# Optimization experiments

Hardware: AMD Instinct MI355X
Metric: run time of the kernel (lower is better)

The kernel has to match this reference:

```python
import jax, jax.numpy as jnp
import numpy as np

WS = 7            # window_size
P = WS * WS       # tokens per window
NUM_HEADS = 12
N_SCALES = 3      # n_local_region_scales
LOCAL_HEAD = NUM_HEADS // N_SCALES

# relative position index (Swin-style), precomputed as a constant
_coords = np.stack(np.meshgrid(np.arange(WS), np.arange(WS), indexing='ij'))  # (2,WS,WS)
_cf = _coords.reshape(2, -1)                                                  # (2,P)
_rel = (_cf[:, :, None] - _cf[:, None, :]).transpose(1, 2, 0)                 # (P,P,2)
_rel[:, :, 0] += WS - 1
_rel[:, :, 1] += WS - 1
_rel[:, :, 0] *= 2 * WS - 1
REL_IDX = jnp.asarray(_rel.sum(-1))  # (P,P) int


def window_partition(arr, ws):
    # arr: (B, H, W, C) -> (B * H/ws * W/ws, ws, ws, C)
    B, H, W, C = arr.shape
    a = arr.reshape(B, H // ws, ws, W // ws, ws, C)
    return a.transpose(0, 1, 3, 2, 4, 5).reshape(-1, ws, ws, C)


def setup_inputs() -> dict:
    key = jax.random.key(0)
    ks = jax.random.split(key, 4)
    B, H, W, C = 16, 56, 56, 384
    N = H * W
    return {
        'x': jax.random.normal(ks[0], (B, N, C), dtype=jnp.float32),
        'w_qkv': jax.random.normal(ks[1], (C, 3 * C), dtype=jnp.float32) * 0.02,
        'w_proj': jax.random.normal(ks[2], (C, C), dtype=jnp.float32) * 0.02,
        'b_proj': jnp.zeros((C,), dtype=jnp.float32),
        'rel_bias_table': jax.random.normal(ks[3], ((2 * WS - 1) ** 2, LOCAL_HEAD), dtype=jnp.float32) * 0.02,
        'H': H,
        'W': W,
    }


def reference(x, w_qkv, w_proj, b_proj, rel_bias_table, H, W):
    B, N, C = x.shape
    head_dim = C // NUM_HEADS
    local_C = C // N_SCALES
    scale = head_dim ** -0.5

    # qkv projection (no bias), laid out as (3, B, N, C)
    temp = (x @ w_qkv).reshape(B, N, 3, C).transpose(2, 0, 1, 3)

    # relative position bias: (LOCAL_HEAD, P, P)
    bias = rel_bias_table[REL_IDX.reshape(-1)].reshape(P, P, LOCAL_HEAD).transpose(2, 0, 1)

    outs = []
    for i in range(N_SCALES):
        qkv = temp[:, :, :, i * local_C:(i + 1) * local_C]          # (3,B,N,local_C)
        oh, ow = H // (2 ** i), W // (2 ** i)
        n_region = (oh // WS) * (ow // WS)
        qkv = qkv.reshape(3 * B, N, local_C).transpose(0, 2, 1).reshape(3 * B, local_C, H, W)
        if i > 0:
            k = 2 ** i
            r = qkv.reshape(3 * B, local_C, oh, k, ow, k)
            qkv = r.mean(axis=(3, 5)) + r.max(axis=(3, 5))           # avg_pool + max_pool
        qkv = qkv.transpose(0, 2, 3, 1)                              # (3B, oh, ow, local_C)
        qkv = window_partition(qkv, WS)                              # (3B*n_region, WS, WS, local_C)
        qkv = qkv.reshape(3, B, n_region, WS, WS, LOCAL_HEAD, head_dim).transpose(0, 1, 5, 2, 3, 4, 6)
        # NOTE: the original reshapes (B,LOCAL_HEAD,n_region,WS,WS,hd) -> (-1,LOCAL_HEAD,P,hd),
        # which mixes batch/head/region axes; replicated faithfully (row-major reshape).
        q = qkv[0].reshape(-1, LOCAL_HEAD, P, head_dim)
        kk = qkv[1].reshape(-1, LOCAL_HEAD, P, head_dim)
        v = qkv[2].reshape(-1, LOCAL_HEAD, P, head_dim)
        attn = (q * scale) @ jnp.swapaxes(kk, -2, -1) + bias[None]   # (B*R, LH, P, P)
        attn = jax.nn.softmax(attn, axis=-1)
        y = attn @ v                                                 # (B*R, LH, P, hd)
        # faithful inverse of the mixed reshape + (non-inverse) window merge via plain reshape
        y = y.reshape(B, n_region, LOCAL_HEAD, P, head_dim).transpose(0, 2, 4, 1, 3)
        y = y.reshape(B, local_C, oh, ow)
        if i > 0:
            y = jax.image.resize(y, (B, local_C, H, W), method='bilinear')
        y = y.reshape(B, LOCAL_HEAD, head_dim, H, W).transpose(0, 1, 3, 4, 2)  # (B,LH,H,W,hd)
        outs.append(y)

    fused = jnp.concatenate(outs, axis=1)                            # (B,NUM_HEADS,H,W,hd)
    fused = fused.reshape(B, NUM_HEADS, N, C // NUM_HEADS).transpose(0, 2, 1, 3).reshape(B, N, C)
    return fused @ w_proj + b_proj
```

## Files before the change

### kernel.cpp

```cpp
#include <hip/hip_runtime.h>
#include <hip/hip_bf16.h>

typedef __hip_bfloat16 bf16;
typedef __hip_bfloat162 bf16x2;
typedef __attribute__((ext_vector_type(8))) short short8;
typedef __attribute__((ext_vector_type(4))) float f32x4;

__device__ __forceinline__ float bf2f(short v) {
  return __uint_as_float(((unsigned)(unsigned short)v) << 16);
}
__device__ __forceinline__ bf16 rawbf(short v) {
  unsigned short b = (unsigned short)v; return *(bf16*)&b;
}
__device__ __forceinline__ void storeOut(float* p, float v) { *p = v; }
__device__ __forceinline__ void storeOut(bf16* p, float v) { *p = __float2bfloat16(v); }

#define GLOAD_LDS16(g, l)                                              \
  __builtin_amdgcn_global_load_lds(                                    \
      (const __attribute__((address_space(1))) void*)(g),              \
      (__attribute__((address_space(3))) void*)(l), 16, 0, 0)

__global__ __launch_bounds__(256) void prep_kernel(const float* __restrict__ x,
                                                   const float* __restrict__ w_qkv,
                                                   const float* __restrict__ w_proj,
                                                   bf16* __restrict__ xb,
                                                   bf16* __restrict__ wqkvT,
                                                   bf16* __restrict__ wprojT)
{
  int bid = blockIdx.x;
  if (bid < 9408) {
    int i = bid * 256 + threadIdx.x;
    const float4* p = (const float4*)x + (size_t)i * 2;
    float4 a = p[0], b = p[1];
    union { short8 v; bf16 h[8]; } u;
    u.h[0] = __float2bfloat16(a.x); u.h[1] = __float2bfloat16(a.y);
    u.h[2] = __float2bfloat16(a.z); u.h[3] = __float2bfloat16(a.w);
    u.h[4] = __float2bfloat16(b.x); u.h[5] = __float2bfloat16(b.y);
    u.h[6] = __float2bfloat16(b.z); u.h[7] = __float2bfloat16(b.w);
    *((short8*)xb + i) = u.v;
  } else {
    int idx = (bid - 9408) * 256 + threadIdx.x;
    if (idx < 1152 * 384) {
      int n = idx / 384, k = idx - n * 384;
      wqkvT[idx] = __float2bfloat16(w_qkv[(size_t)k * 1152 + n]);
    } else {
      idx -= 1152 * 384;
      int n = idx / 384, k = idx - n * 384;
      wprojT[idx] = __float2bfloat16(w_proj[(size_t)k * 384 + n]);
    }
  }
}

template<typename TC, bool BIAS>
__global__ __launch_bounds__(512) void gemm_mfma(const bf16* __restrict__ A,
                                                 const bf16* __restrict__ Bt,
                                                 const float* __restrict__ bias,
                                                 TC* __restrict__ C,
                                                 int M, int N, int K, int nbx)
{
  __shared__ __align__(16) bf16 As[256 * 64];
  __shared__ __align__(16) bf16 Bs[128 * 64];
  const int tid = threadIdx.x;
  const int wave = tid >> 6, lane = tid & 63;
  const int nwg = gridDim.x;
  const int qc = nwg >> 3, rr = nwg & 7;
  const int xcd = blockIdx.x & 7, jj = blockIdx.x >> 3;
  const int wg = (xcd < rr ? xcd * (qc + 1) : rr * (qc + 1) + (xcd - rr) * qc) + jj;
  const int by = wg / nbx, bx = wg - by * nbx;
  const int bm = by * 256, bn = bx * 128;
  const int wr = wave >> 1, wc = wave & 1;

  f32x4 acc[4][4] = {};

  const bf16* aP[4];
  const bf16* bP[2];
#pragma unroll
  for (int e = 0; e < 4; ++e) {
    int flat = e * 8192 + tid * 16;
    int r = flat >> 7;
    int q = ((flat >> 4) & 7) ^ (r & 7);
    aP[e] = A + (size_t)(bm + r) * K + q * 8;
  }
#pragma unroll
  for (int e = 0; e < 2; ++e) {
    int flat = e * 8192 + tid * 16;
    int r = flat >> 7;
    int q = ((flat >> 4) & 7) ^ (r & 7);
    bP[e] = Bt + (size_t)(bn + r) * K + q * 8;
  }
  char* AsW = (char*)As + wave * 1024;
  char* BsW = (char*)Bs + wave * 1024;

  const int lr = lane & 15, lk = lane >> 4;
  const int rbA = (wr * 64 + lr) * 64;
  const int rbB = (wc * 64 + lr) * 64;
  const int q0 = ((lk    ) ^ (lr & 7)) * 8;
  const int q1 = ((4 + lk) ^ (lr & 7)) * 8;

  for (int k0 = 0; k0 < K; k0 += 64) {
#pragma unroll
    for (int e = 0; e < 4; ++e) GLOAD_LDS16(aP[e] + k0, AsW + e * 8192);
#pragma unroll
    for (int e = 0; e < 2; ++e) GLOAD_LDS16(bP[e] + k0, BsW + e * 8192);
    __syncthreads();
    short8 af0[4], af1[4], bf0[4], bf1[4];
#pragma unroll
    for (int i = 0; i < 4; ++i) {
      af0[i] = *(const short8*)(As + rbA + i * 1024 + q0);
      af1[i] = *(const short8*)(As + rbA + i * 1024 + q1);
    }
#pragma unroll
    for (int j = 0; j < 4; ++j) {
      bf0[j] = *(const short8*)(Bs + rbB + j * 1024 + q0);
      bf1[j] = *(const short8*)(Bs + rbB + j * 1024 + q1);
    }
#pragma unroll
    for (int i = 0; i < 4; ++i)
#pragma unroll
      for (int j = 0; j < 4; ++j) {
        acc[i][j] = __builtin_amdgcn_mfma_f32_16x16x32_bf16(af0[i], bf0[j], acc[i][j], 0, 0, 0);
        acc[i][j] = __builtin_amdgcn_mfma_f32_16x16x32_bf16(af1[i], bf1[j], acc[i][j], 0, 0, 0);
      }
    __syncthreads();
  }

  const int crow = bm + wr * 64 + lk * 4;
  const int ccol = bn + wc * 64 + lr;
#pragma unroll
  for (int j = 0; j < 4; ++j) {
    int col = ccol + j * 16;
    float bv = BIAS ? bias[col] : 0.f;
#pragma unroll
    for (int i = 0; i < 4; ++i)
#pragma unroll
      for (int t = 0; t < 4; ++t) {
        int row = crow + i * 16 + t;
        storeOut(&C[(size_t)row * N + col], acc[i][j][t] + bv);
      }
  }
}

template<typename TC, bool BIAS>
__global__ __launch_bounds__(256) void gemm128(const bf16* __restrict__ A,
                                               const bf16* __restrict__ Bt,
                                               const float* __restrict__ bias,
                                               TC* __restrict__ C,
                                               int M, int N, int K, int nbx)
{
  __shared__ __align__(16) bf16 As[128 * 64];
  __shared__ __align__(16) bf16 Bs[128 * 64];
  const int tid = threadIdx.x;
  const int wave = tid >> 6, lane = tid & 63;
  const int cpx = gridDim.x >> 3;
  const int wg = (blockIdx.x & 7) * cpx + (blockIdx.x >> 3);
  const int by = wg / nbx, bx = wg - by * nbx;
  const int bm = by * 128, bn = bx * 128;
  const int wr = wave >> 1, wc = wave & 1;

  f32x4 acc[4][4] = {};

  const bf16* aP[4];
  const bf16* bP[4];
#pragma unroll
  for (int e = 0; e < 4; ++e) {
    int flat = e * 4096 + tid * 16;
    int r = flat >> 7;
    int q = ((flat >> 4) & 7) ^ (r & 7);
    aP[e] = A + (size_t)(bm + r) * K + q * 8;
    bP[e] = Bt + (size_t)(bn + r) * K + q * 8;
  }
  char* AsW = (char*)As + wave * 1024;
  char* BsW = (char*)Bs + wave * 1024;

  const int lr = lane & 15, lk = lane >> 4;
  const int rbA = (wr * 64 + lr) * 64;
  const int rbB = (wc * 64 + lr) * 64;
  const int q0 = ((lk    ) ^ (lr & 7)) * 8;
  const int q1 = ((4 + lk) ^ (lr & 7)) * 8;

  for (int k0 = 0; k0 < K; k0 += 64) {
#pragma unroll
    for (int e = 0; e < 4; ++e) GLOAD_LDS16(aP[e] + k0, AsW + e * 4096);
#pragma unroll
    for (int e = 0; e < 4; ++e) GLOAD_LDS16(bP[e] + k0, BsW + e * 4096);
    __syncthreads();
    short8 af0[4], af1[4], bf0[4], bf1[4];
#pragma unroll
    for (int i = 0; i < 4; ++i) {
      af0[i] = *(const short8*)(As + rbA + i * 1024 + q0);
      af1[i] = *(const short8*)(As + rbA + i * 1024 + q1);
    }
#pragma unroll
    for (int j = 0; j < 4; ++j) {
      bf0[j] = *(const short8*)(Bs + rbB + j * 1024 + q0);
      bf1[j] = *(const short8*)(Bs + rbB + j * 1024 + q1);
    }
#pragma unroll
    for (int i = 0; i < 4; ++i)
#pragma unroll
      for (int j = 0; j < 4; ++j) {
        acc[i][j] = __builtin_amdgcn_mfma_f32_16x16x32_bf16(af0[i], bf0[j], acc[i][j], 0, 0, 0);
        acc[i][j] = __builtin_amdgcn_mfma_f32_16x16x32_bf16(af1[i], bf1[j], acc[i][j], 0, 0, 0);
      }
    __syncthreads();
  }

  const int crow = bm + wr * 64 + lk * 4;
  const int ccol = bn + wc * 64 + lr;
#pragma unroll
  for (int j = 0; j < 4; ++j) {
    int col = ccol + j * 16;
    float bv = BIAS ? bias[col] : 0.f;
#pragma unroll
    for (int i = 0; i < 4; ++i)
#pragma unroll
      for (int t = 0; t < 4; ++t) {
        int row = crow + i * 16 + t;
        storeOut(&C[(size_t)row * N + col], acc[i][j][t] + bv);
      }
  }
}

struct AttnP {
  const bf16 *qb, *kb, *vb;
  bf16* out;
  int R, Rw, f, npos, out_cstride, out_coffset, blk0;
};

template<int F>
__device__ __forceinline__ void attn_body(const float* __restrict__ btable,
                                          const AttnP& p, int blk,
                                          bf16* KP, bf16* Vt, float* bias_s)
{
  const int b = blk / p.R, r = blk % p.R;
  const int rh = r / p.Rw, rw = r % p.Rw;
  const int tid = threadIdx.x;
  const int h = tid >> 6, lane = tid & 63;
  const int lr = lane & 15, lk = lane >> 4;
  const int hb = r & 3;
  const float pinv = 1.0f / (float)(F * F);

  if (tid < 169) bias_s[tid] = btable[tid * 4 + hb];

  const size_t gbase = (size_t)b * 3136 * 1152;

#pragma unroll
  for (int c0 = 0; c0 < 4; ++c0) {
    int j = c0 * 256 + tid;
    if (j < 784) {
      int row = j >> 4, r4 = j & 15;
      int hh = r4 >> 2, slot = r4 & 3;
      int r7 = (row * 9363) >> 16, rm = row - r7 * 7;
      const bf16* src = p.kb + gbase +
          ((size_t)((rh * 7 + r7) * F) * 56 + (rw * 7 + rm) * F) * 1152 + hh * 32 + slot * 8;
      short8 ov;
      if (F == 1) {
        ov = *(const short8*)src;
      } else {
        float sum[8] = {}, mx[8];
#pragma unroll
        for (int e = 0; e < 8; ++e) mx[e] = -3.4e38f;
#pragma unroll
        for (int dy = 0; dy < F; ++dy)
#pragma unroll
          for (int dx = 0; dx < F; ++dx) {
            short8 v = *(const short8*)(src + ((size_t)dy * 56 + dx) * 1152);
#pragma unroll
            for (int e = 0; e < 8; ++e) {
              float fv = bf2f(v[e]); sum[e] += fv; mx[e] = fmaxf(mx[e], fv);
            }
          }
        union { short8 v; bf16 hb8[8]; } u;
#pragma unroll
        for (int e = 0; e < 8; ++e) u.hb8[e] = __float2bfloat16(sum[e] * pinv + mx[e]);
        ov = u.v;
      }
      *(short8*)(KP + hh * 4096 + row * 40 + slot * 8) = ov;
    }
  }

#pragma unroll
  for (int c0 = 0; c0 < 4; ++c0) {
    int j = c0 * 256 + tid;
    int pp = j >> 4, r4 = j & 15;
    int hh = r4 >> 2, d8 = r4 & 3;
    bf16 hv[8];
    if (pp < 49) {
      int r7 = (pp * 9363) >> 16, rm = pp - r7 * 7;
      const bf16* src = p.vb + gbase +
          ((size_t)((rh * 7 + r7) * F) * 56 + (rw * 7 + rm) * F) * 1152 + hh * 32 + d8 * 8;
      if (F == 1) {
        short8 v = *(const short8*)src;
#pragma unroll
        for (int e = 0; e < 8; ++e) hv[e] = rawbf(v[e]);
      } else {
        float sum[8] = {}, mx[8];
#pragma unroll
        for (int e = 0; e < 8; ++e) mx[e] = -3.4e38f;
#pragma unroll
        for (int dy = 0; dy < F; ++dy)
#pragma unroll
          for (int dx = 0; dx < F; ++dx) {
            short8 v = *(const short8*)(src + ((size_t)dy * 56 + dx) * 1152);
#pragma unroll
            for (int e = 0; e < 8; ++e) {
              float fv = bf2f(v[e]); sum[e] += fv; mx[e] = fmaxf(mx[e], fv);
            }
          }
#pragma unroll
        for (int e = 0; e < 8; ++e) hv[e] = __float2bfloat16(sum[e] * pinv + mx[e]);
      }
    } else {
#pragma unroll
      for (int e = 0; e < 8; ++e) hv[e] = __float2bfloat16(0.f);
    }
#pragma unroll
    for (int e = 0; e < 8; ++e) {
      int d = d8 * 8 + e;
      Vt[hh * 2048 + d * 64 + ((pp >> 3) ^ (d & 7)) * 8 + (pp & 7)] = hv[e];
    }
  }

  short8 qa[4];
#pragma unroll
  for (int it = 0; it < 4; ++it) {
    int pq = it * 16 + lr; pq = min(pq, 48);
    int r7 = (pq * 9363) >> 16, rm = pq - r7 * 7;
    const bf16* src = p.qb + gbase +
        ((size_t)((rh * 7 + r7) * F) * 56 + (rw * 7 + rm) * F) * 1152 + h * 32 + lk * 8;
    if (F == 1) {
      qa[it] = *(const short8*)src;
    } else {
      float sum[8] = {}, mx[8];
#pragma unroll
      for (int e = 0; e < 8; ++e) mx[e] = -3.4e38f;
#pragma unroll
      for (int dy = 0; dy < F; ++dy)
#pragma unroll
        for (int dx = 0; dx < F; ++dx) {
          short8 v = *(const short8*)(src + ((size_t)dy * 56 + dx) * 1152);
#pragma unroll
          for (int e = 0; e < 8; ++e) {
            float fv = bf2f(v[e]); sum[e] += fv; mx[e] = fmaxf(mx[e], fv);
          }
        }
      union { short8 v; bf16 hb8[8]; } u;
#pragma unroll
      for (int e = 0; e < 8; ++e) u.hb8[e] = __float2bfloat16(sum[e] * pinv + mx[e]);
      qa[it] = u.v;
    }
  }

  __syncthreads();

  f32x4 s[4][4];
  {
    short8 kf[4];
#pragma unroll
    for (int jt = 0; jt < 4; ++jt)
      kf[jt] = *(const short8*)(KP + h * 4096 + (jt * 16 + lr) * 40 + lk * 8);
    const f32x4 z = {0.f, 0.f, 0.f, 0.f};
    __builtin_amdgcn_s_setprio(1);
#pragma unroll
    for (int it = 0; it < 4; ++it)
#pragma unroll
      for (int jt = 0; jt < 4; ++jt)
        s[it][jt] = __builtin_amdgcn_mfma_f32_16x16x32_bf16(qa[it], kf[jt], z, 0, 0, 0);
    __builtin_amdgcn_s_setprio(0);
  }

  const float scale = 0.17677669529663687f;
  const bool colpad = (lr != 0);
  int pp7[4], ppm[4];
#pragma unroll
  for (int jt = 0; jt < 4; ++jt) {
    int pp = min(jt * 16 + lr, 48);
    pp7[jt] = (pp * 9363) >> 16; ppm[jt] = pp - pp7[jt] * 7;
  }
  float sm[4][4];
#pragma unroll
  for (int it = 0; it < 4; ++it)
#pragma unroll
    for (int t = 0; t < 4; ++t) {
      int pq = min(it * 16 + lk * 4 + t, 48);
      int q7 = (pq * 9363) >> 16, qm = pq - q7 * 7;
#pragma unroll
      for (int jt = 0; jt < 4; ++jt) {
        float bv = bias_s[(q7 - pp7[jt] + 6) * 13 + (qm - ppm[jt] + 6)];
        float v = fmaf(s[it][jt][t], scale, bv);
        if (jt == 3 && colpad) v = -1e30f;
        s[it][jt][t] = v;
      }
      float m = fmaxf(fmaxf(s[it][0][t], s[it][1][t]), fmaxf(s[it][2][t], s[it][3][t]));
      m = fmaxf(m, __shfl_xor(m, 1));
      m = fmaxf(m, __shfl_xor(m, 2));
      m = fmaxf(m, __shfl_xor(m, 4));
      m = fmaxf(m, __shfl_xor(m, 8));
      float ssum = 0.f;
#pragma unroll
      for (int jt = 0; jt < 4; ++jt) {
        float e = __expf(s[it][jt][t] - m);
        s[it][jt][t] = e; ssum += e;
      }
      ssum += __shfl_xor(ssum, 1);
      ssum += __shfl_xor(ssum, 2);
      ssum += __shfl_xor(ssum, 4);
      ssum += __shfl_xor(ssum, 8);
      sm[it][t] = 1.0f / ssum;
    }

#pragma unroll
  for (int it = 0; it < 4; ++it)
#pragma unroll
    for (int t = 0; t < 4; ++t) {
      int prow = it * 16 + lk * 4 + t;
#pragma unroll
      for (int jt = 0; jt < 4; ++jt) {
        int slot = (jt * 2 + (lr >> 3)) ^ (prow & 7);
        KP[h * 4096 + prow * 64 + slot * 8 + (lr & 7)] = __float2bfloat16(s[it][jt][t]);
      }
    }
  __syncthreads();

  f32x4 o[4][2] = {};
#pragma unroll
  for (int ks = 0; ks < 2; ++ks) {
    short8 pf[4], vf[2];
#pragma unroll
    for (int it = 0; it < 4; ++it) {
      int prow = it * 16 + lr;
      pf[it] = *(const short8*)(KP + h * 4096 + prow * 64 + ((ks * 4 + lk) ^ (prow & 7)) * 8);
    }
#pragma unroll
    for (int jd = 0; jd < 2; ++jd) {
      int d = jd * 16 + lr;
      vf[jd] = *(const short8*)(Vt + h * 2048 + d * 64 + ((ks * 4 + lk) ^ (d & 7)) * 8);
    }
    __builtin_amdgcn_s_setprio(1);
#pragma unroll
    for (int it = 0; it < 4; ++it)
#pragma unroll
      for (int jd = 0; jd < 2; ++jd)
        o[it][jd] = __builtin_amdgcn_mfma_f32_16x16x32_bf16(pf[it], vf[jd], o[it][jd], 0, 0, 0);
    __builtin_amdgcn_s_setprio(0);
  }

  const int c0 = (r & 3) * 32;
#pragma unroll
  for (int it = 0; it < 4; ++it)
#pragma unroll
    for (int t = 0; t < 4; ++t) {
      int prow = it * 16 + lk * 4 + t;
      if (prow < 49) {
        int m_out = (h * (p.R >> 2) + (r >> 2)) * 49 + prow;
        bf16* op = p.out + ((size_t)b * p.npos + m_out) * p.out_cstride + p.out_coffset + c0;
#pragma unroll
        for (int jd = 0; jd < 2; ++jd)
          op[jd * 16 + lr] = __float2bfloat16(o[it][jd][t] * sm[it][t]);
      }
    }
}

__global__ __launch_bounds__(256) void attn_mfma(const float* __restrict__ btable,
                                                 AttnP P0, AttnP P1, AttnP P2)
{
  __shared__ __align__(16) bf16 KP[4 * 4096];
  __shared__ __align__(16) bf16 Vt[4 * 2048];
  __shared__ float bias_s[169];

  const AttnP p = (blockIdx.x >= (unsigned)P0.blk0) ? P0
                : (blockIdx.x >= (unsigned)P1.blk0) ? P1 : P2;
  const int blk = blockIdx.x - p.blk0;
  if (p.f == 1)      attn_body<1>(btable, p, blk, KP, Vt, bias_s);
  else if (p.f == 2) attn_body<2>(btable, p, blk, KP, Vt, bias_s);
  else               attn_body<4>(btable, p, blk, KP, Vt, bias_s);
}

__device__ __forceinline__ float2 bilerp2(const bf16* __restrict__ base, int dim, int h, int w, int cp)
{
  float r = (float)dim / 56.f;
  float uy = (h + 0.5f) * r - 0.5f;
  float ux = (w + 0.5f) * r - 0.5f;
  float fy0 = floorf(uy), fx0 = floorf(ux);
  int y0 = (int)fy0, x0 = (int)fx0;
  float fy = uy - fy0, fx = ux - fx0;
  int y0c = max(y0, 0), y1c = min(y0 + 1, dim - 1);
  int x0c = max(x0, 0), x1c = min(x0 + 1, dim - 1);
  bf16x2 v00 = *(const bf16x2*)(base + ((size_t)y0c * dim + x0c) * 128 + cp * 2);
  bf16x2 v01 = *(const bf16x2*)(base + ((size_t)y0c * dim + x1c) * 128 + cp * 2);
  bf16x2 v10 = *(const bf16x2*)(base + ((size_t)y1c * dim + x0c) * 128 + cp * 2);
  bf16x2 v11 = *(const bf16x2*)(base + ((size_t)y1c * dim + x1c) * 128 + cp * 2);
  float w00 = (1.f - fy) * (1.f - fx), w01 = (1.f - fy) * fx;
  float w10 = fy * (1.f - fx),        w11 = fy * fx;
  float2 o;
  o.x = w00 * __bfloat162float(v00.x) + w01 * __bfloat162float(v01.x) +
        w10 * __bfloat162float(v10.x) + w11 * __bfloat162float(v11.x);
  o.y = w00 * __bfloat162float(v00.y) + w01 * __bfloat162float(v01.y) +
        w10 * __bfloat162float(v10.y) + w11 * __bfloat162float(v11.y);
  return o;
}

__global__ __launch_bounds__(256) void upsample_both_kernel(const bf16* __restrict__ yb1,
                                                            const bf16* __restrict__ yb2,
                                                            bf16* __restrict__ fused)
{
  int t = blockIdx.x * 256 + threadIdx.x;
  int cp = t & 63;
  int pos = t >> 6;
  int n = pos % 3136, b = pos / 3136;
  int h = n / 56, w = n % 56;
  float2 s1 = bilerp2(yb1 + (size_t)b * 784 * 128, 28, h, w, cp);
  float2 s2 = bilerp2(yb2 + (size_t)b * 196 * 128, 14, h, w, cp);
  bf16* op = fused + (size_t)pos * 384;
  bf16x2 o1; o1.x = __float2bfloat16(s1.x); o1.y = __float2bfloat16(s1.y);
  bf16x2 o2; o2.x = __float2bfloat16(s2.x); o2.y = __float2bfloat16(s2.y);
  *(bf16x2*)(op + 128 + cp * 2) = o1;
  *(bf16x2*)(op + 256 + cp * 2) = o2;
}

extern "C" void kernel_launch(void* const* d_in, const int* in_sizes, int n_in,
                              void* d_out, int out_size, void* d_ws, size_t ws_size,
                              hipStream_t stream)
{
  const float* x      = (const float*)d_in[0];
  const float* w_qkv  = (const float*)d_in[1];
  const float* w_proj = (const float*)d_in[2];
  const float* b_proj = (const float*)d_in[3];
  const float* btable = (const float*)d_in[4];

  bf16* temp  = (bf16*)d_ws;
  bf16* fused = temp  + (size_t)50176 * 1152 + (size_t)3 * 16 * 980 * 128;
  bf16* ybuf1 = fused + (size_t)50176 * 384;
  bf16* ybuf2 = ybuf1 + (size_t)16 * 784 * 128;
  bf16* wqkvT = ybuf2 + (size_t)16 * 196 * 128;
  bf16* wprojT= wqkvT + (size_t)1152 * 384;
  bf16* xb    = fused;

  prep_kernel<<<9408 + 2304, 256, 0, stream>>>(x, w_qkv, w_proj, xb, wqkvT, wprojT);

  gemm_mfma<bf16, false><<<1764, 512, 0, stream>>>(
      xb, wqkvT, nullptr, temp, 50176, 1152, 384, 9);

  AttnP P2{temp + 256, temp + 640, temp + 1024, ybuf2,
           4, 2, 4, 196, 128, 0, 0};
  AttnP P1{temp + 128, temp + 512, temp + 896, ybuf1,
           16, 4, 2, 784, 128, 0, 64};
  AttnP P0{temp, temp + 384, temp + 768, fused,
           64, 8, 1, 3136, 384, 0, 320};
  attn_mfma<<<1344, 256, 0, stream>>>(btable, P0, P1, P2);

  upsample_both_kernel<<<16 * 3136 * 64 / 256, 256, 0, stream>>>(ybuf1, ybuf2, fused);

  gemm128<float, true><<<1176, 256, 0, stream>>>(
      fused, wprojT, b_proj, (float*)d_out, 50176, 384, 384, 3);
}
```

Measured before the change: 174.3 us.

## Commute bilinear upsample with output projection and fuse into proj GEMM epilogue

Since bilinear resize is linear, the scale-1 and scale-2 attention outputs are projected through their slices of w_proj at low resolution (small GEMMs producing z1/z2). The main projection GEMM now runs with K=128 over only the full-resolution channels. Its epilogue stages the tile in LDS and adds bias plus bilinearly interpolated z1/z2 rows, which removes the separate upsample kernel and two thirds of the big GEMM's K work. It costs two extra launches and eight gathered 16-byte loads per output chunk in the epilogue. The projected values are rounded to bf16 before interpolation, so rounding differs slightly from the original order.

```diff
diff --git a/kernel.cpp b/kernel.cpp
--- a/kernel.cpp
+++ b/kernel.cpp
@@ -140,19 +140,42 @@
   }
 }
 
-template<typename TC, bool BIAS>
-__global__ __launch_bounds__(256) void gemm128(const bf16* __restrict__ A,
-                                               const bf16* __restrict__ Bt,
+__device__ __forceinline__ void bilerp_setup(int dim, int h, int w,
+                                             int& r00, int& r01, int& r10, int& r11,
+                                             float& w00, float& w01, float& w10, float& w11)
+{
+  float r = (float)dim / 56.f;
+  float uy = (h + 0.5f) * r - 0.5f;
+  float ux = (w + 0.5f) * r - 0.5f;
+  float fy0 = floorf(uy), fx0 = floorf(ux);
+  int y0 = (int)fy0, x0 = (int)fx0;
+  float fy = uy - fy0, fx = ux - fx0;
+  int y0c = max(y0, 0), y1c = min(y0 + 1, dim - 1);
+  int x0c = max(x0, 0), x1c = min(x0 + 1, dim - 1);
+  w00 = (1.f - fy) * (1.f - fx); w01 = (1.f - fy) * fx;
+  w10 = fy * (1.f - fx);        w11 = fy * fx;
+  r00 = y0c * dim + x0c; r01 = y0c * dim + x1c;
+  r10 = y1c * dim + x0c; r11 = y1c * dim + x1c;
+}
+
+template<typename TC, bool EPI>
+__global__ __launch_bounds__(256) void gemm128(const bf16* __restrict__ A, int lda,
+                                               const bf16* __restrict__ Bt, int ldb,
                                                const float* __restrict__ bias,
+                                               const bf16* __restrict__ z1,
+                                               const bf16* __restrict__ z2,
                                                TC* __restrict__ C,
                                                int M, int N, int K, int nbx)
 {
-  __shared__ __align__(16) bf16 As[128 * 64];
-  __shared__ __align__(16) bf16 Bs[128 * 64];
+  __shared__ __align__(16) bf16 smem[128 * 128];
+  bf16* As = smem;
+  bf16* Bs = smem + 128 * 64;
   const int tid = threadIdx.x;
   const int wave = tid >> 6, lane = tid & 63;
-  const int cpx = gridDim.x >> 3;
-  const int wg = (blockIdx.x & 7) * cpx + (blockIdx.x >> 3);
+  const int nwg = gridDim.x;
+  const int qc = nwg >> 3, rr = nwg & 7;
+  const int xcd = blockIdx.x & 7, jj0 = blockIdx.x >> 3;
+  const int wg = (xcd < rr ? xcd * (qc + 1) : rr * (qc + 1) + (xcd - rr) * qc) + jj0;
   const int by = wg / nbx, bx = wg - by * nbx;
   const int bm = by * 128, bn = bx * 128;
   const int wr = wave >> 1, wc = wave & 1;
@@ -166,8 +189,8 @@
     int flat = e * 4096 + tid * 16;
     int r = flat >> 7;
     int q = ((flat >> 4) & 7) ^ (r & 7);
-    aP[e] = A + (size_t)(bm + r) * K + q * 8;
-    bP[e] = Bt + (size_t)(bn + r) * K + q * 8;
+    aP[e] = A + (size_t)(bm + r) * lda + q * 8;
+    bP[e] = Bt + (size_t)(bn + r) * ldb + q * 8;
   }
   char* AsW = (char*)As + wave * 1024;
   char* BsW = (char*)Bs + wave * 1024;
@@ -205,19 +228,74 @@
     __syncthreads();
   }
 
-  const int crow = bm + wr * 64 + lk * 4;
-  const int ccol = bn + wc * 64 + lr;
-#pragma unroll
-  for (int j = 0; j < 4; ++j) {
-    int col = ccol + j * 16;
-    float bv = BIAS ? bias[col] : 0.f;
+  if (!EPI) {
+    const int crow = bm + wr * 64 + lk * 4;
+    const int ccol = bn + wc * 64 + lr;
+#pragma unroll
+    for (int j = 0; j < 4; ++j) {
+      int col = ccol + j * 16;
+#pragma unroll
+      for (int i = 0; i < 4; ++i)
+#pragma unroll
+        for (int t = 0; t < 4; ++t) {
+          int row = crow + i * 16 + t;
+          storeOut(&C[(size_t)row * N + col], acc[i][j][t]);
+        }
+    }
+  } else {
 #pragma unroll
     for (int i = 0; i < 4; ++i)
 #pragma unroll
       for (int t = 0; t < 4; ++t) {
-        int row = crow + i * 16 + t;
-        storeOut(&C[(size_t)row * N + col], acc[i][j][t] + bv);
-      }
+        int rl = wr * 64 + lk * 4 + i * 16 + t;
+#pragma unroll
+        for (int j = 0; j < 4; ++j) {
+          int cl = wc * 64 + j * 16 + lr;
+          int ss = (cl >> 3) ^ (rl & 15);
+          smem[rl * 128 + ss * 8 + (cl & 7)] = __float2bfloat16(acc[i][j][t]);
+        }
+      }
+    __syncthreads();
+    float* outC = (float*)C;
+#pragma unroll
+    for (int jj = 0; jj < 8; ++jj) {
+      int job = jj * 256 + tid;
+      int rl = job >> 4, cg = job & 15;
+      int m = bm + rl;
+      int col0 = bn + cg * 8;
+      short8 av = *(const short8*)(smem + rl * 128 + ((cg ^ (rl & 15)) * 8));
+      int bI = m / 3136, n = m - bI * 3136;
+      int h = n / 56, w = n - h * 56;
+      int a00, a01, a10, a11; float w00, w01, w10, w11;
+      bilerp_setup(28, h, w, a00, a01, a10, a11, w00, w01, w10, w11);
+      int c00, c01, c10, c11; float v00, v01, v10, v11;
+      bilerp_setup(14, h, w, c00, c01, c10, c11, v00, v01, v10, v11);
+      const bf16* z1b = z1 + (size_t)bI * 784 * 384 + col0;
+      const bf16* z2b = z2 + (size_t)bI * 196 * 384 + col0;
+      short8 Z00 = *(const short8*)(z1b + (size_t)a00 * 384);
+      short8 Z01 = *(const short8*)(z1b + (size_t)a01 * 384);
+      short8 Z10 = *(const short8*)(z1b + (size_t)a10 * 384);
+      short8 Z11 = *(const short8*)(z1b + (size_t)a11 * 384);
+      short8 Y00 = *(const short8*)(z2b + (size_t)c00 * 384);
+      short8 Y01 = *(const short8*)(z2b + (size_t)c01 * 384);
+      short8 Y10 = *(const short8*)(z2b + (size_t)c10 * 384);
+      short8 Y11 = *(const short8*)(z2b + (size_t)c11 * 384);
+      float4 b0 = *(const float4*)(bias + col0);
+      float4 b1 = *(const float4*)(bias + col0 + 4);
+      float bb[8] = {b0.x, b0.y, b0.z, b0.w, b1.x, b1.y, b1.z, b1.w};
+      float outv[8];
+#pragma unroll
+      for (int e = 0; e < 8; ++e) {
+        outv[e] = bf2f(av[e]) + bb[e]
+                + w00 * bf2f(Z00[e]) + w01 * bf2f(Z01[e])
+                + w10 * bf2f(Z10[e]) + w11 * bf2f(Z11[e])
+                + v00 * bf2f(Y00[e]) + v01 * bf2f(Y01[e])
+                + v10 * bf2f(Y10[e]) + v11 * bf2f(Y11[e]);
+      }
+      float* op = outC + (size_t)m * N + col0;
+      *(float4*)op       = make_float4(outv[0], outv[1], outv[2], outv[3]);
+      *(float4*)(op + 4) = make_float4(outv[4], outv[5], outv[6], outv[7]);
+    }
   }
 }
 
@@ -476,48 +554,6 @@
   else               attn_body<4>(btable, p, blk, KP, Vt, bias_s);
 }
 
-__device__ __forceinline__ float2 bilerp2(const bf16* __restrict__ base, int dim, int h, int w, int cp)
-{
-  float r = (float)dim / 56.f;
-  float uy = (h + 0.5f) * r - 0.5f;
-  float ux = (w + 0.5f) * r - 0.5f;
-  float fy0 = floorf(uy), fx0 = floorf(ux);
-  int y0 = (int)fy0, x0 = (int)fx0;
-  float fy = uy - fy0, fx = ux - fx0;
-  int y0c = max(y0, 0), y1c = min(y0 + 1, dim - 1);
-  int x0c = max(x0, 0), x1c = min(x0 + 1, dim - 1);
-  bf16x2 v00 = *(const bf16x2*)(base + ((size_t)y0c * dim + x0c) * 128 + cp * 2);
-  bf16x2 v01 = *(const bf16x2*)(base + ((size_t)y0c * dim + x1c) * 128 + cp * 2);
-  bf16x2 v10 = *(const bf16x2*)(base + ((size_t)y1c * dim + x0c) * 128 + cp * 2);
-  bf16x2 v11 = *(const bf16x2*)(base + ((size_t)y1c * dim + x1c) * 128 + cp * 2);
-  float w00 = (1.f - fy) * (1.f - fx), w01 = (1.f - fy) * fx;
-  float w10 = fy * (1.f - fx),        w11 = fy * fx;
-  float2 o;
-  o.x = w00 * __bfloat162float(v00.x) + w01 * __bfloat162float(v01.x) +
-        w10 * __bfloat162float(v10.x) + w11 * __bfloat162float(v11.x);
-  o.y = w00 * __bfloat162float(v00.y) + w01 * __bfloat162float(v01.y) +
-        w10 * __bfloat162float(v10.y) + w11 * __bfloat162float(v11.y);
-  return o;
-}
-
-__global__ __launch_bounds__(256) void upsample_both_kernel(const bf16* __restrict__ yb1,
-                                                            const bf16* __restrict__ yb2,
-                                                            bf16* __restrict__ fused)
-{
-  int t = blockIdx.x * 256 + threadIdx.x;
-  int cp = t & 63;
-  int pos = t >> 6;
-  int n = pos % 3136, b = pos / 3136;
-  int h = n / 56, w = n % 56;
-  float2 s1 = bilerp2(yb1 + (size_t)b * 784 * 128, 28, h, w, cp);
-  float2 s2 = bilerp2(yb2 + (size_t)b * 196 * 128, 14, h, w, cp);
-  bf16* op = fused + (size_t)pos * 384;
-  bf16x2 o1; o1.x = __float2bfloat16(s1.x); o1.y = __float2bfloat16(s1.y);
-  bf16x2 o2; o2.x = __float2bfloat16(s2.x); o2.y = __float2bfloat16(s2.y);
-  *(bf16x2*)(op + 128 + cp * 2) = o1;
-  *(bf16x2*)(op + 256 + cp * 2) = o2;
-}
-
 extern "C" void kernel_launch(void* const* d_in, const int* in_sizes, int n_in,
                               void* d_out, int out_size, void* d_ws, size_t ws_size,
                               hipStream_t stream)
@@ -529,10 +565,12 @@
   const float* btable = (const float*)d_in[4];
 
   bf16* temp  = (bf16*)d_ws;
-  bf16* fused = temp  + (size_t)50176 * 1152 + (size_t)3 * 16 * 980 * 128;
+  bf16* fused = temp  + (size_t)50176 * 1152;
   bf16* ybuf1 = fused + (size_t)50176 * 384;
   bf16* ybuf2 = ybuf1 + (size_t)16 * 784 * 128;
-  bf16* wqkvT = ybuf2 + (size_t)16 * 196 * 128;
+  bf16* z1    = ybuf2 + (size_t)16 * 196 * 128;
+  bf16* z2    = z1    + (size_t)12544 * 384;
+  bf16* wqkvT = z2    + (size_t)3200 * 384;
   bf16* wprojT= wqkvT + (size_t)1152 * 384;
   bf16* xb    = fused;
 
@@ -549,8 +587,14 @@
            64, 8, 1, 3136, 384, 0, 320};
   attn_mfma<<<1344, 256, 0, stream>>>(btable, P0, P1, P2);
 
-  upsample_both_kernel<<<16 * 3136 * 64 / 256, 256, 0, stream>>>(ybuf1, ybuf2, fused);
+  gemm128<bf16, false><<<294, 256, 0, stream>>>(
+      ybuf1, 128, wprojT + 128, 384, nullptr, nullptr, nullptr,
+      z1, 12544, 384, 128, 3);
+  gemm128<bf16, false><<<75, 256, 0, stream>>>(
+      ybuf2, 128, wprojT + 256, 384, nullptr, nullptr, nullptr,
+      z2, 3200, 384, 128, 3);
 
   gemm128<float, true><<<1176, 256, 0, stream>>>(
-      fused, wprojT, b_proj, (float*)d_out, 50176, 384, 384, 3);
-}
+      fused, 384, wprojT, 384, b_proj, z1, z2,
+      (float*)d_out, 50176, 384, 128, 3);
+}
```

After: 190.4 us. +9.2%, slower.
